# Kernel optimization log

Hardware: AMD Instinct MI355X
Metric: run time of the kernel (lower is better)

Reference implementation:

```python
import jax, jax.numpy as jnp
import numpy as np

B, L, D, H, K = 64, 512, 768, 768, 128


def setup_inputs() -> dict:
    key = jax.random.key(0)
    ks = jax.random.split(key, 8)
    enc = jax.random.normal(ks[0], (B, L, D), dtype=jnp.float32)
    valid_mask = jax.random.randint(ks[1], (B, L), 0, 2)
    pos_span = jnp.sort(jax.random.randint(ks[2], (B, 2), 0, 40), axis=-1)
    mask_span = jax.random.randint(ks[3], (B,), 0, L)
    s1 = 1.0 / np.sqrt(D)
    s2 = 1.0 / np.sqrt(H)
    W1 = jax.random.normal(ks[4], (D, H), dtype=jnp.float32) * s1
    b1 = jax.random.normal(ks[5], (H,), dtype=jnp.float32) * s1
    W2 = jax.random.normal(ks[6], (H, K), dtype=jnp.float32) * s2
    b2 = jax.random.normal(ks[7], (K,), dtype=jnp.float32) * s2
    return {"encoder_layers": enc, "W1": W1, "b1": b1, "W2": W2, "b2": b2,
            "valid_mask": valid_mask, "pos_span": pos_span, "mask_span": mask_span}


def _pretrained_feature(enc, valid_mask, pos_span, mask_span):
    # mask_feat: gather token at mask_span[i] per row -> [B, D]
    mask_feat = enc[jnp.arange(B), mask_span]
    # Compact valid tokens to the front of each row (stable order).
    v = valid_mask == 1                               # [B, L]
    pos = jnp.cumsum(v.astype(jnp.int32), axis=1) - 1  # compacted dest index
    dest = jnp.where(v, pos, L)                        # invalid tokens -> slot L (dropped)
    valid_output = jnp.zeros((B, L + 1, D), dtype=enc.dtype)
    valid_output = valid_output.at[jnp.arange(B)[:, None], dest].set(enc)
    valid_output = valid_output[:, :L]                 # rest stays zero, as in torch
    # Span-wise max pool over compacted positions [start, end] inclusive.
    p = jnp.arange(L)[None, :]
    span = (p >= pos_span[:, 0:1]) & (p <= pos_span[:, 1:2])  # [B, L]
    neg_inf = jnp.array(-jnp.inf, dtype=enc.dtype)
    feat = jnp.max(jnp.where(span[:, :, None], valid_output, neg_inf), axis=1)
    return feat, mask_feat


def reference(encoder_layers, W1, b1, W2, b2, valid_mask, pos_span, mask_span):
    feat, _mask_feat = _pretrained_feature(encoder_layers, valid_mask, pos_span, mask_span)
    # head: Linear -> ReLU -> Dropout(eval: identity) -> Linear
    h = jax.nn.relu(feat @ W1 + b1)
    logits = h @ W2 + b2
    return logits
```

## Files before the change

kernel.cpp:

```cpp
#include <hip/hip_runtime.h>
#include <math.h>

#define BB 64
#define LL 512
#define DD 768
#define HH 768
#define KK 128

static __device__ __forceinline__ float4 fmax4(float4 a, float4 b) {
    float4 r;
    r.x = fmaxf(a.x, b.x); r.y = fmaxf(a.y, b.y);
    r.z = fmaxf(a.z, b.z); r.w = fmaxf(a.w, b.w);
    return r;
}

__global__ __launch_bounds__(1024, 1) void halton_featmlp_kernel(
    const float* __restrict__ enc,
    const float* __restrict__ W1,
    const float* __restrict__ b1,
    const int*   __restrict__ valid_mask,
    const int*   __restrict__ pos_span,
    float*       __restrict__ h)
{
    __shared__ int    s_idx[4][40];
    __shared__ int    s_count[4];
    __shared__ float4 s_red[4][4][192];
    __shared__ float  s_feat[4][DD];
    __shared__ float  s_part[16][4][64];

    const int tid   = threadIdx.x;
    const int jbase = blockIdx.x * 64;
    const int bbase = blockIdx.y * 4;
    const int lane  = tid & 63;
    const int w     = tid >> 6;
    const int j     = jbase + lane;

    const float rb1 = b1[jbase + lane];
    const int   kp  = w * 48;
    float w0p = W1[(kp + 0) * HH + j];
    float w1p = W1[(kp + 1) * HH + j];
    float w2p = W1[(kp + 2) * HH + j];
    float w3p = W1[(kp + 3) * HH + j];
    const int bl_g = w & 3;
    const int g_g  = w >> 2;
    const int bgat = bbase + bl_g;
    const int lo   = pos_span[bgat * 2 + 0];
    const int hi   = pos_span[bgat * 2 + 1];

    if (w < 4) {
        const int b = bbase + w;
        int v[8];
        #pragma unroll
        for (int c = 0; c < 8; ++c)
            v[c] = valid_mask[b * LL + c * 64 + lane];
        int count = 0;
        #pragma unroll
        for (int c = 0; c < 8; ++c) {
            unsigned long long mk = __ballot(v[c] == 1);
            if (v[c] == 1) {
                int rank = count + __popcll(mk & ((1ull << lane) - 1ull));
                if (rank < 40) s_idx[w][rank] = c * 64 + lane;
            }
            count += __popcll(mk);
        }
        if (lane == 0) s_count[w] = count;
    }
    __syncthreads();

    {
        const int count = s_count[bl_g];
        const int pend  = min(hi, count - 1);

        const float4 ninf = make_float4(-INFINITY, -INFINITY, -INFINITY, -INFINITY);
        float4 m0 = ninf, m1 = ninf, m2 = ninf;
        float4 n0 = ninf, n1 = ninf, n2 = ninf;
        for (int p = lo + g_g; p <= pend; p += 8) {
            const float4* r4 = (const float4*)&enc[((long)bgat * LL + s_idx[bl_g][p]) * DD];
            m0 = fmax4(m0, r4[lane]);
            m1 = fmax4(m1, r4[lane + 64]);
            m2 = fmax4(m2, r4[lane + 128]);
            if (p + 4 <= pend) {
                const float4* q4 = (const float4*)&enc[((long)bgat * LL + s_idx[bl_g][p + 4]) * DD];
                n0 = fmax4(n0, q4[lane]);
                n1 = fmax4(n1, q4[lane + 64]);
                n2 = fmax4(n2, q4[lane + 128]);
            }
        }
        m0 = fmax4(m0, n0); m1 = fmax4(m1, n1); m2 = fmax4(m2, n2);
        if (hi >= count) {
            const float4 z = make_float4(0.f, 0.f, 0.f, 0.f);
            m0 = fmax4(m0, z); m1 = fmax4(m1, z); m2 = fmax4(m2, z);
        }
        s_red[g_g][bl_g][lane]       = m0;
        s_red[g_g][bl_g][lane + 64]  = m1;
        s_red[g_g][bl_g][lane + 128] = m2;
    }
    __syncthreads();

    if (lane < 48) {
        const int bl = lane / 12;
        const int kf = w * 12 + lane % 12;
        float4 r = fmax4(fmax4(s_red[0][bl][kf], s_red[1][bl][kf]),
                         fmax4(s_red[2][bl][kf], s_red[3][bl][kf]));
        ((float4*)&s_feat[bl][0])[kf] = r;
    }

    {
        const float4* f40 = (const float4*)&s_feat[0][0];
        const float4* f41 = (const float4*)&s_feat[1][0];
        const float4* f42 = (const float4*)&s_feat[2][0];
        const float4* f43 = (const float4*)&s_feat[3][0];

        float a0, a1, a2, a3;
        {
            const int kf = w * 12;
            const float4 fv0 = f40[kf], fv1 = f41[kf], fv2 = f42[kf], fv3 = f43[kf];
            a0 = fv0.x * w0p + fv0.y * w1p + fv0.z * w2p + fv0.w * w3p;
            a1 = fv1.x * w0p + fv1.y * w1p + fv1.z * w2p + fv1.w * w3p;
            a2 = fv2.x * w0p + fv2.y * w1p + fv2.z * w2p + fv2.w * w3p;
            a3 = fv3.x * w0p + fv3.y * w1p + fv3.z * w2p + fv3.w * w3p;
        }
        #pragma unroll 4
        for (int k4 = 1; k4 < 12; ++k4) {
            const int kf = w * 12 + k4;
            const int k  = kf * 4;
            const float4 fv0 = f40[kf];
            const float4 fv1 = f41[kf];
            const float4 fv2 = f42[kf];
            const float4 fv3 = f43[kf];
            const float w0 = W1[(k + 0) * HH + j];
            const float w1 = W1[(k + 1) * HH + j];
            const float w2 = W1[(k + 2) * HH + j];
            const float w3 = W1[(k + 3) * HH + j];
            a0 += fv0.x * w0 + fv0.y * w1 + fv0.z * w2 + fv0.w * w3;
            a1 += fv1.x * w0 + fv1.y * w1 + fv1.z * w2 + fv1.w * w3;
            a2 += fv2.x * w0 + fv2.y * w1 + fv2.z * w2 + fv2.w * w3;
            a3 += fv3.x * w0 + fv3.y * w1 + fv3.z * w2 + fv3.w * w3;
        }
        s_part[w][0][lane] = a0;
        s_part[w][1][lane] = a1;
        s_part[w][2][lane] = a2;
        s_part[w][3][lane] = a3;
    }
    __syncthreads();

    if (tid < 256) {
        const int bl  = tid >> 6;
        const int col = tid & 63;
        float r = rb1;
        #pragma unroll
        for (int q = 0; q < 16; ++q) r += s_part[q][bl][col];
        h[(long)(bbase + bl) * HH + jbase + col] = fmaxf(r, 0.f);
    }
}

__global__ __launch_bounds__(384) void halton_gemm2_kernel(
    const float* __restrict__ h,
    const float* __restrict__ W2,
    const float* __restrict__ b2,
    float*       __restrict__ out)
{
    __shared__ float s_part[12][32];

    const int tid = threadIdx.x;
    const int b   = blockIdx.y;
    const int col = blockIdx.x * 32 + (tid & 31);
    const int seg = tid >> 5;

    const float rb2 = b2[col];
    const float4* h4 = (const float4*)&h[(long)b * HH + seg * 64];

    float a0 = 0.f, a1 = 0.f, a2 = 0.f, a3 = 0.f;
    #pragma unroll 4
    for (int i4 = 0; i4 < 16; ++i4) {
        const float4 hv = h4[i4];
        const int k = seg * 64 + i4 * 4;
        a0 += hv.x * W2[(k + 0) * KK + col];
        a1 += hv.y * W2[(k + 1) * KK + col];
        a2 += hv.z * W2[(k + 2) * KK + col];
        a3 += hv.w * W2[(k + 3) * KK + col];
    }
    s_part[seg][tid & 31] = (a0 + a1) + (a2 + a3);
    __syncthreads();

    if (tid < 32) {
        float r = rb2;
        #pragma unroll
        for (int q = 0; q < 12; ++q) r += s_part[q][tid];
        out[b * KK + col] = r;
    }
}

extern "C" void kernel_launch(void* const* d_in, const int* in_sizes, int n_in,
                              void* d_out, int out_size, void* d_ws, size_t ws_size,
                              hipStream_t stream) {
    const float* enc        = (const float*)d_in[0];
    const float* W1         = (const float*)d_in[1];
    const float* b1         = (const float*)d_in[2];
    const float* W2         = (const float*)d_in[3];
    const float* b2         = (const float*)d_in[4];
    const int*   valid_mask = (const int*)d_in[5];
    const int*   pos_span   = (const int*)d_in[6];
    float* out = (float*)d_out;
    float* h   = (float*)d_ws;

    halton_featmlp_kernel<<<dim3(12, 16), 1024, 0, stream>>>(enc, W1, b1,
                                                             valid_mask, pos_span, h);
    halton_gemm2_kernel<<<dim3(4, BB), 384, 0, stream>>>(h, W2, b2, out);
}
```

Before: 18.84 us.

## Fuse second linear layer into feature/MLP kernel with flag-based cross-block reduction

Merges the two kernels into one. Each block computes its 64-column slice of the hidden activation, applies the matching rows of W2 to produce partial logits, and writes them to workspace. The jt==0 block in each batch tile spin-waits on per-block release flags, sums the 12 partials with b2, writes the output, and resets the flags. This removes the second launch and the global round-trip of h. In exchange it depends on all 192 blocks being co-resident to avoid deadlock, and the spin-wait can serialise on the slowest block.

```diff
diff --git a/kernel.cpp b/kernel.cpp
--- a/kernel.cpp
+++ b/kernel.cpp
@@ -6,6 +6,7 @@
 #define DD 768
 #define HH 768
 #define KK 128
+#define FLAG_MAGIC 0x0BADF00D
 
 static __device__ __forceinline__ float4 fmax4(float4 a, float4 b) {
     float4 r;
@@ -14,28 +15,38 @@
     return r;
 }
 
-__global__ __launch_bounds__(1024, 1) void halton_featmlp_kernel(
+__global__ __launch_bounds__(1024, 1) void halton_one_kernel(
     const float* __restrict__ enc,
     const float* __restrict__ W1,
     const float* __restrict__ b1,
+    const float* __restrict__ W2,
+    const float* __restrict__ b2,
     const int*   __restrict__ valid_mask,
     const int*   __restrict__ pos_span,
-    float*       __restrict__ h)
+    float*       __restrict__ out,
+    float*       __restrict__ ws_partial,
+    int*         __restrict__ ws_flags)
 {
     __shared__ int    s_idx[4][40];
     __shared__ int    s_count[4];
     __shared__ float4 s_red[4][4][192];
     __shared__ float  s_feat[4][DD];
     __shared__ float  s_part[16][4][64];
+    __shared__ float  s_hh[4][64];
+    __shared__ float  s_ep[8][128];
 
     const int tid   = threadIdx.x;
-    const int jbase = blockIdx.x * 64;
-    const int bbase = blockIdx.y * 4;
+    const int jt    = blockIdx.x;
+    const int bt    = blockIdx.y;
+    const int jbase = jt * 64;
+    const int bbase = bt * 4;
     const int lane  = tid & 63;
     const int w     = tid >> 6;
     const int j     = jbase + lane;
 
     const float rb1 = b1[jbase + lane];
+    float rb2 = 0.f;
+    if (jt == 0 && tid < 512) rb2 = b2[tid & 127];
     const int   kp  = w * 48;
     float w0p = W1[(kp + 0) * HH + j];
     float w1p = W1[(kp + 1) * HH + j];
@@ -150,44 +161,65 @@
         float r = rb1;
         #pragma unroll
         for (int q = 0; q < 16; ++q) r += s_part[q][bl][col];
-        h[(long)(bbase + bl) * HH + jbase + col] = fmaxf(r, 0.f);
-    }
-}
-
-__global__ __launch_bounds__(384) void halton_gemm2_kernel(
-    const float* __restrict__ h,
-    const float* __restrict__ W2,
-    const float* __restrict__ b2,
-    float*       __restrict__ out)
-{
-    __shared__ float s_part[12][32];
-
-    const int tid = threadIdx.x;
-    const int b   = blockIdx.y;
-    const int col = blockIdx.x * 32 + (tid & 31);
-    const int seg = tid >> 5;
-
-    const float rb2 = b2[col];
-    const float4* h4 = (const float4*)&h[(long)b * HH + seg * 64];
-
-    float a0 = 0.f, a1 = 0.f, a2 = 0.f, a3 = 0.f;
-    #pragma unroll 4
-    for (int i4 = 0; i4 < 16; ++i4) {
-        const float4 hv = h4[i4];
-        const int k = seg * 64 + i4 * 4;
-        a0 += hv.x * W2[(k + 0) * KK + col];
-        a1 += hv.y * W2[(k + 1) * KK + col];
-        a2 += hv.z * W2[(k + 2) * KK + col];
-        a3 += hv.w * W2[(k + 3) * KK + col];
-    }
-    s_part[seg][tid & 31] = (a0 + a1) + (a2 + a3);
-    __syncthreads();
-
-    if (tid < 32) {
-        float r = rb2;
-        #pragma unroll
-        for (int q = 0; q < 12; ++q) r += s_part[q][tid];
-        out[b * KK + col] = r;
+        s_hh[bl][col] = fmaxf(r, 0.f);
+    }
+    __syncthreads();
+
+    {
+        const int col2 = tid & 127;
+        const int bl   = (tid >> 7) & 3;
+        const int kh   = tid >> 9;
+        float a0 = 0.f, a1 = 0.f, a2 = 0.f, a3 = 0.f;
+        #pragma unroll 8
+        for (int i = 0; i < 32; i += 4) {
+            const int k0 = kh * 32 + i;
+            a0 += s_hh[bl][k0 + 0] * W2[(jbase + k0 + 0) * KK + col2];
+            a1 += s_hh[bl][k0 + 1] * W2[(jbase + k0 + 1) * KK + col2];
+            a2 += s_hh[bl][k0 + 2] * W2[(jbase + k0 + 2) * KK + col2];
+            a3 += s_hh[bl][k0 + 3] * W2[(jbase + k0 + 3) * KK + col2];
+        }
+        s_ep[(bl << 1) | kh][col2] = (a0 + a1) + (a2 + a3);
+    }
+    __syncthreads();
+
+    if (tid < 512) {
+        const int bl  = tid >> 7;
+        const int col = tid & 127;
+        const float p = s_ep[bl * 2][col] + s_ep[bl * 2 + 1][col];
+        __hip_atomic_store(&ws_partial[((bt * 12 + jt) * 4 + bl) * 128 + col], p,
+                           __ATOMIC_RELAXED, __HIP_MEMORY_SCOPE_AGENT);
+    }
+    __syncthreads();
+    if (tid == 0)
+        __hip_atomic_store(&ws_flags[bt * 12 + jt], (int)FLAG_MAGIC,
+                           __ATOMIC_RELEASE, __HIP_MEMORY_SCOPE_AGENT);
+
+    if (jt == 0) {
+        if (w == 0) {
+            bool done;
+            do {
+                int f = (lane < 12)
+                    ? __hip_atomic_load(&ws_flags[bt * 12 + lane],
+                                        __ATOMIC_ACQUIRE, __HIP_MEMORY_SCOPE_AGENT)
+                    : (int)FLAG_MAGIC;
+                done = __all(f == (int)FLAG_MAGIC);
+            } while (!done);
+        }
+        __syncthreads();
+
+        if (tid < 512) {
+            const int bl  = tid >> 7;
+            const int col = tid & 127;
+            float r = rb2;
+            #pragma unroll
+            for (int q = 0; q < 12; ++q)
+                r += __hip_atomic_load(&ws_partial[((bt * 12 + q) * 4 + bl) * 128 + col],
+                                       __ATOMIC_RELAXED, __HIP_MEMORY_SCOPE_AGENT);
+            out[(bbase + bl) * KK + col] = r;
+        }
+        if (tid < 12)
+            __hip_atomic_store(&ws_flags[bt * 12 + tid], 0,
+                               __ATOMIC_RELAXED, __HIP_MEMORY_SCOPE_AGENT);
     }
 }
 
@@ -201,10 +233,10 @@
     const float* b2         = (const float*)d_in[4];
     const int*   valid_mask = (const int*)d_in[5];
     const int*   pos_span   = (const int*)d_in[6];
-    float* out = (float*)d_out;
-    float* h   = (float*)d_ws;
-
-    halton_featmlp_kernel<<<dim3(12, 16), 1024, 0, stream>>>(enc, W1, b1,
-                                                             valid_mask, pos_span, h);
-    halton_gemm2_kernel<<<dim3(4, BB), 384, 0, stream>>>(h, W2, b2, out);
+    float* out        = (float*)d_out;
+    float* ws_partial = (float*)d_ws;
+    int*   ws_flags   = (int*)d_ws + 16 * 12 * 4 * 128;
+
+    halton_one_kernel<<<dim3(12, 16), 1024, 0, stream>>>(
+        enc, W1, b1, W2, b2, valid_mask, pos_span, out, ws_partial, ws_flags);
 }
```

Result: no change. 18.98 us (+0.7%).
